# Performance work log

Hardware: AMD Instinct MI355X
Metric: run time of the kernel (lower is better)

Reference implementation:

```python
import jax, jax.numpy as jnp
import numpy as np

HIDDEN = 1024
HEADS = 16
HEAD_DIM = HIDDEN // HEADS
B, T = 4, 2048


def setup_inputs() -> dict:
    key = jax.random.key(0)
    k_x, k_w1, k_b1, k_w2, k_b2 = jax.random.split(key, 5)
    lim1 = 1.0 / np.sqrt(HIDDEN)
    x = jax.random.normal(k_x, (B, T, HIDDEN), dtype=jnp.float32)
    # causal lower-triangular mask, broadcastable to [B, H, T, T]
    mask = jnp.tril(jnp.ones((T, T), dtype=jnp.int32))[None, None, :, :]
    # qkv_proj: Linear(HIDDEN, 3*HIDDEN); torch Linear: y = x @ W.T + b
    W_qkv = jax.random.uniform(k_w1, (3 * HIDDEN, HIDDEN), minval=-lim1, maxval=lim1, dtype=jnp.float32)
    b_qkv = jax.random.uniform(k_b1, (3 * HIDDEN,), minval=-lim1, maxval=lim1, dtype=jnp.float32)
    W_out = jax.random.uniform(k_w2, (HIDDEN, HIDDEN), minval=-lim1, maxval=lim1, dtype=jnp.float32)
    b_out = jax.random.uniform(k_b2, (HIDDEN,), minval=-lim1, maxval=lim1, dtype=jnp.float32)
    return {"x": x, "mask": mask, "W_qkv": W_qkv, "b_qkv": b_qkv, "W_out": W_out, "b_out": b_out}


def reference(x, mask, W_qkv, b_qkv, W_out, b_out):
    Bx, Tx, C = x.shape
    qkv = x @ W_qkv.T + b_qkv                      # [B, T, 3C]
    qkv = qkv.reshape(Bx, Tx, 3, HEADS, HEAD_DIM)
    qkv = jnp.transpose(qkv, (2, 0, 3, 1, 4))      # [3, B, H, T, Dh]
    Q, K, V = qkv[0], qkv[1], qkv[2]
    scale = 1.0 / np.sqrt(HEAD_DIM)
    scores = jnp.einsum('bhqd,bhkd->bhqk', Q, K) * scale  # [B, H, T, T]
    scores = jnp.where(mask == 0, -jnp.inf, scores)
    probs = jax.nn.softmax(scores, axis=-1)
    ctx = jnp.einsum('bhqk,bhkd->bhqd', probs, V)  # [B, H, T, Dh]
    ctx = jnp.transpose(ctx, (0, 2, 1, 3)).reshape(Bx, Tx, C)
    return ctx @ W_out.T + b_out
```

## Files before the change

kernel.cpp:

```cpp
#include <hip/hip_runtime.h>
#include <cstdint>
#include <cstddef>

#define B_ 4
#define T_ 2048
#define C_ 1024
#define H_ 16
#define D_ 64

typedef __attribute__((ext_vector_type(8))) __bf16 bf16x8;
typedef __attribute__((ext_vector_type(4))) float floatx4;

#define QSCL (0.125f * 1.44269504088896f)
#define FMAX 24.0f

__device__ __forceinline__ unsigned short f2bf(float f) {
  union { float f; unsigned int u; } v; v.f = f;
  unsigned int r = v.u + 0x7fffu + ((v.u >> 16) & 1u);
  return (unsigned short)(r >> 16);
}
__device__ __forceinline__ ushort4 pk4(float a, float b, float c, float d) {
  ushort4 u; u.x = f2bf(a); u.y = f2bf(b); u.z = f2bf(c); u.w = f2bf(d);
  return u;
}
__device__ __forceinline__ bf16x8 cvt8(float4 a, float4 b) {
  bf16x8 r;
  r[0] = a.x; r[1] = a.y; r[2] = a.z; r[3] = a.w;
  r[4] = b.x; r[5] = b.y; r[6] = b.z; r[7] = b.w;
  return r;
}
__device__ __forceinline__ ushort4 pk4c(float a, float b, float c, float d) {
  union { __bf16 b4[4]; ushort4 u; } w;
  w.b4[0] = (__bf16)a; w.b4[1] = (__bf16)b; w.b4[2] = (__bf16)c; w.b4[3] = (__bf16)d;
  return w.u;
}

__device__ __forceinline__ void gl_lds16(const void* g, void* l) {
  __builtin_amdgcn_global_load_lds(
      (const __attribute__((address_space(1))) unsigned int*)g,
      (__attribute__((address_space(3))) unsigned int*)l, 16, 0, 0);
}

__global__ __launch_bounds__(256)
void conv_bf16(const float* __restrict__ src, unsigned short* __restrict__ dst,
               int n8) {
  for (int i = blockIdx.x * 256 + threadIdx.x; i < n8; i += gridDim.x * 256) {
    const float4* s = (const float4*)src + 2 * (size_t)i;
    float4 a = s[0], b = s[1];
    ((bf16x8*)dst)[i] = cvt8(a, b);
  }
}

__global__ __launch_bounds__(256)
void conv_tri(const float* __restrict__ s1, unsigned short* __restrict__ d1, int n1,
              const float* __restrict__ s2, unsigned short* __restrict__ d2, int n2,
              const float* __restrict__ s3, unsigned short* __restrict__ d3, int n3) {
  for (int i = blockIdx.x * 256 + threadIdx.x; i < n1 + n2 + n3; i += gridDim.x * 256) {
    const float4* sp; bf16x8* dp;
    if (i < n1)           { sp = (const float4*)s1 + 2 * (size_t)i;       dp = (bf16x8*)d1 + i; }
    else if (i < n1 + n2) { int j = i - n1;      sp = (const float4*)s2 + 2 * (size_t)j; dp = (bf16x8*)d2 + j; }
    else                  { int j = i - n1 - n2; sp = (const float4*)s3 + 2 * (size_t)j; dp = (bf16x8*)d3 + j; }
    float4 a = sp[0], b = sp[1];
    *dp = cvt8(a, b);
  }
}

template<int EPI, int GATHER, int WBF>
__global__ __launch_bounds__(256, 3)
void gemm_bt(const unsigned short* __restrict__ Abf,
             const void* __restrict__ Wraw,
             const float* __restrict__ bias,
             float* __restrict__ out,
             unsigned short* __restrict__ qws,
             unsigned short* __restrict__ kws,
             unsigned short* __restrict__ vtws)
{
  alignas(16) __shared__ unsigned short As[128 * 64];
  alignas(16) __shared__ unsigned short Bs[WBF ? 128 * 64 : 128 * 72];
  const int tid  = threadIdx.x;
  const int lane = tid & 63;
  const int wid  = tid >> 6;
  const int col  = lane & 15;
  const int quad = lane >> 4;
  const int wm = (wid >> 1) << 6;
  const int wn = (wid & 1) << 6;
  const int bm = blockIdx.y << 7;
  const int bn = blockIdx.x << 7;

  const float* Wf          = (const float*)Wraw;
  const unsigned short* Wb = (const unsigned short*)Wraw;

  const int r0 = tid >> 3;
  const int c0 = tid & 7;

  floatx4 acc[4][4];
#pragma unroll
  for (int i = 0; i < 4; ++i)
#pragma unroll
    for (int j = 0; j < 4; ++j)
      acc[i][j] = (floatx4){0.f, 0.f, 0.f, 0.f};

  for (int k0 = 0; k0 < 1024; k0 += 64) {
    __syncthreads();
#pragma unroll
    for (int s = 0; s < 4; ++s) {
      const int row  = (s << 5) + r0;
      const int colE = ((c0 ^ (row & 7)) << 3);
      const unsigned short* gsrc;
      if (GATHER) {
        const int m = bm + row;
        const int b = m >> 11, t = m & 2047;
        const int h = k0 >> 6;
        gsrc = Abf + ((((size_t)(b * 16 + h) << 11) + t) << 6) + colE;
      } else {
        gsrc = Abf + (size_t)(bm + row) * 1024 + k0 + colE;
      }
      gl_lds16(gsrc, (char*)As + (s << 12) + (wid << 10));
    }
    if (WBF) {
#pragma unroll
      for (int s = 0; s < 4; ++s) {
        const int row  = (s << 5) + r0;
        const int colE = ((c0 ^ (row & 7)) << 3);
        const unsigned short* gsrc = Wb + (size_t)(bn + row) * 1024 + k0 + colE;
        gl_lds16(gsrc, (char*)Bs + (s << 12) + (wid << 10));
      }
    } else {
#pragma unroll
      for (int s = 0; s < 4; ++s) {
        const int row = (s << 5) + r0;
        const int kc  = c0 << 3;
        const float* wsrc = &Wf[(size_t)(bn + row) * 1024 + k0 + kc];
        float4 w0 = *(const float4*)wsrc;
        float4 w1 = *(const float4*)(wsrc + 4);
        *(bf16x8*)&Bs[row * 72 + kc] = cvt8(w0, w1);
      }
    }
    __syncthreads();
#pragma unroll
    for (int kk = 0; kk < 64; kk += 32) {
      bf16x8 af[4], bfr[4];
#pragma unroll
      for (int i = 0; i < 4; ++i) {
        const int r = wm + i * 16 + col;
        af[i] = *(const bf16x8*)&As[(r << 6) + ((kk + quad * 8) ^ ((r & 7) << 3))];
      }
#pragma unroll
      for (int j = 0; j < 4; ++j) {
        const int r = wn + j * 16 + col;
        if (WBF)
          bfr[j] = *(const bf16x8*)&Bs[(r << 6) + ((kk + quad * 8) ^ ((r & 7) << 3))];
        else
          bfr[j] = *(const bf16x8*)&Bs[r * 72 + kk + quad * 8];
      }
#pragma unroll
      for (int i = 0; i < 4; ++i)
#pragma unroll
        for (int j = 0; j < 4; ++j)
          acc[i][j] = __builtin_amdgcn_mfma_f32_16x16x32_bf16(af[i], bfr[j], acc[i][j], 0, 0, 0);
    }
  }

#pragma unroll
  for (int i = 0; i < 4; ++i) {
    const int row = bm + wm + i * 16 + quad * 4;
#pragma unroll
    for (int j = 0; j < 4; ++j) {
      const int n  = bn + wn + j * 16 + col;
      const float bv = bias[n];
      float v[4];
#pragma unroll
      for (int r = 0; r < 4; ++r) v[r] = acc[i][j][r] + bv;

      if (EPI == 1) {
#pragma unroll
        for (int r = 0; r < 4; ++r)
          out[(size_t)(row + r) * 1024 + n] = v[r];
      } else {
        const int s   = n >> 10;
        const int rem = n & 1023;
        const int h   = rem >> 6;
        const int d   = rem & 63;
        const int b   = row >> 11;
        const int t   = row & 2047;
        const size_t bh = (size_t)(b * H_ + h);
        if (s == 0) {
#pragma unroll
          for (int r = 0; r < 4; ++r)
            qws[(bh * T_ + t + r) * D_ + d] = f2bf(v[r] * QSCL);
        } else if (s == 1) {
#pragma unroll
          for (int r = 0; r < 4; ++r)
            kws[(bh * T_ + t + r) * D_ + d] = f2bf(v[r]);
        } else {
          *(ushort4*)&vtws[(bh * D_ + d) * T_ + t] = pk4(v[0], v[1], v[2], v[3]);
        }
      }
    }
  }
}

__global__ __launch_bounds__(256, 3)
void attn_causal(unsigned short* __restrict__ qws,
                 const unsigned short* __restrict__ kws,
                 const unsigned short* __restrict__ vtws)
{
  alignas(16) __shared__ unsigned short Ks[2][64 * 64];
  alignas(16) __shared__ unsigned short Vs[2][64 * 64];
  alignas(16) __shared__ unsigned short Ps[4][2][16][72];
  const int tid  = threadIdx.x;
  const int lane = tid & 63;
  const int wid  = tid >> 6;
  const int col  = lane & 15;
  const int quad = lane >> 4;

  const int bh   = blockIdx.x & 63;
  const int band = 15 - (blockIdx.x >> 6);

  const unsigned short* Kp  = kws + (size_t)bh * T_ * D_;
  const unsigned short* Vtp = vtws + (size_t)bh * D_ * T_;

  bf16x8 vones;
#pragma unroll
  for (int i = 0; i < 8; ++i) vones[i] = (__bf16)1.0f;

  const int srow8 = lane >> 3;
  const int swz   = ((lane & 7) ^ srow8) << 3;

#define STAGE(kt_, b_)                                                        \
  do {                                                                        \
    _Pragma("unroll") for (int c2 = 0; c2 < 2; ++c2) {                        \
      const int cb = wid + (c2 << 2);                   \
      gl_lds16(Kp + ((size_t)(((kt_) << 6) + (cb << 3) + srow8) << 6) + swz,  \
               (char*)&Ks[b_][0] + (cb << 10));                               \
      gl_lds16(Vtp + ((size_t)((cb << 3) + srow8) << 11) + ((kt_) << 6) + swz,\
               (char*)&Vs[b_][0] + (cb << 10));                               \
    }                                                                         \
  } while (0)

  const int nk = (band << 1) + 2;
  const int q0 = (band << 7) + (wid << 5);
  unsigned short* Qp = qws + ((size_t)bh * T_ + q0) * D_;

  bf16x8 bq[2][2];
#pragma unroll
  for (int h = 0; h < 2; ++h) {
    bq[h][0] = *(const bf16x8*)&Qp[(h * 16 + col) * D_ + quad * 8];
    bq[h][1] = *(const bf16x8*)&Qp[(h * 16 + col) * D_ + 32 + quad * 8];
  }

  floatx4 o[2][4], ol[2];
#pragma unroll
  for (int h = 0; h < 2; ++h) {
    ol[h] = (floatx4){0.f, 0.f, 0.f, 0.f};
#pragma unroll
    for (int j = 0; j < 4; ++j) o[h][j] = (floatx4){0.f, 0.f, 0.f, 0.f};
  }

  STAGE(0, 0);
  __syncthreads();

  for (int kt = 0; kt < nk; ++kt) {
    const int buf = kt & 1;
    if (kt + 1 < nk) STAGE(kt + 1, buf ^ 1);

    const unsigned short* Kb = &Ks[buf][0];
    bf16x8 kA[4], kB[4];
#pragma unroll
    for (int g = 0; g < 4; ++g) {
      const int r = g * 16 + col;
      kA[g] = *(const bf16x8*)&Kb[(r << 6) + ((quad ^ (col & 7)) << 3)];
      kB[g] = *(const bf16x8*)&Kb[(r << 6) + (((quad | 4) ^ (col & 7)) << 3)];
    }

    floatx4 s[2][4];
    __builtin_amdgcn_s_setprio(1);
#pragma unroll
    for (int h = 0; h < 2; ++h)
#pragma unroll
      for (int g = 0; g < 4; ++g) {
        s[h][g] = (floatx4){-FMAX, -FMAX, -FMAX, -FMAX};
        s[h][g] = __builtin_amdgcn_mfma_f32_16x16x32_bf16(kA[g], bq[h][0], s[h][g], 0, 0, 0);
        s[h][g] = __builtin_amdgcn_mfma_f32_16x16x32_bf16(kB[g], bq[h][1], s[h][g], 0, 0, 0);
      }
    __builtin_amdgcn_s_setprio(0);

    if (kt >= nk - 2) {
#pragma unroll
      for (int h = 0; h < 2; ++h) {
        const int lim = q0 - (kt << 6) + (h << 4) + col;
#pragma unroll
        for (int g = 0; g < 4; ++g)
#pragma unroll
          for (int r = 0; r < 4; ++r)
            if (g * 16 + quad * 4 + r > lim) s[h][g][r] = -1e30f;
      }
    }

#pragma unroll
    for (int h = 0; h < 2; ++h)
#pragma unroll
      for (int g = 0; g < 4; ++g)
#pragma unroll
        for (int r = 0; r < 4; ++r)
          s[h][g][r] = exp2f(s[h][g][r]);

#pragma unroll
    for (int h = 0; h < 2; ++h)
#pragma unroll
      for (int g = 0; g < 4; ++g)
        *(ushort4*)&Ps[wid][h][col][g * 16 + quad * 4] =
            pk4c(s[h][g][0], s[h][g][1], s[h][g][2], s[h][g][3]);
    asm volatile("s_waitcnt lgkmcnt(0)" ::: "memory");

    const unsigned short* Vb = &Vs[buf][0];
    bf16x8 vA[4], vB[4];
#pragma unroll
    for (int j = 0; j < 4; ++j) {
      const int r = j * 16 + col;
      vA[j] = *(const bf16x8*)&Vb[(r << 6) + ((quad ^ (col & 7)) << 3)];
      vB[j] = *(const bf16x8*)&Vb[(r << 6) + (((quad | 4) ^ (col & 7)) << 3)];
    }

    __builtin_amdgcn_s_setprio(1);
#pragma unroll
    for (int h = 0; h < 2; ++h) {
      const bf16x8 ap0 = *(const bf16x8*)&Ps[wid][h][col][quad * 8];
      const bf16x8 ap1 = *(const bf16x8*)&Ps[wid][h][col][32 + quad * 8];
#pragma unroll
      for (int j = 0; j < 4; ++j) {
        o[h][j] = __builtin_amdgcn_mfma_f32_16x16x32_bf16(ap0, vA[j], o[h][j], 0, 0, 0);
        o[h][j] = __builtin_amdgcn_mfma_f32_16x16x32_bf16(ap1, vB[j], o[h][j], 0, 0, 0);
      }
      ol[h] = __builtin_amdgcn_mfma_f32_16x16x32_bf16(ap0, vones, ol[h], 0, 0, 0);
      ol[h] = __builtin_amdgcn_mfma_f32_16x16x32_bf16(ap1, vones, ol[h], 0, 0, 0);
    }
    __builtin_amdgcn_s_setprio(0);

    __syncthreads();
  }

#pragma unroll
  for (int h = 0; h < 2; ++h) {
    float lr[4];
#pragma unroll
    for (int r = 0; r < 4; ++r) lr[r] = 1.0f / ol[h][r];
#pragma unroll
    for (int j = 0; j < 4; ++j)
#pragma unroll
      for (int r = 0; r < 4; ++r)
        Qp[(size_t)(h * 16 + quad * 4 + r) * D_ + j * 16 + col] =
            f2bf(o[h][j][r] * lr[r]);
  }
#undef STAGE
}

extern "C" void kernel_launch(void* const* d_in, const int* in_sizes, int n_in,
                              void* d_out, int out_size, void* d_ws, size_t ws_size,
                              hipStream_t stream) {
  const float* x     = (const float*)d_in[0];
  const float* W_qkv = (const float*)d_in[2];
  const float* b_qkv = (const float*)d_in[3];
  const float* W_out = (const float*)d_in[4];
  const float* b_out = (const float*)d_in[5];
  float* out = (float*)d_out;

  const size_t per = (size_t)B_ * H_ * T_ * D_;
  unsigned short* qws  = (unsigned short*)d_ws;
  unsigned short* vtws = qws + per;
  unsigned short* kws  = (unsigned short*)d_out;
  unsigned short* xbf  = kws + per;

  const bool bigws  = ws_size >= (size_t)38 * 1024 * 1024;
  const bool hugews = ws_size >= (size_t)40 * 1024 * 1024;
  unsigned short* wqbf = vtws + per;
  unsigned short* wobf = wqbf + (size_t)3 * C_ * C_;

  if (hugews) {
    conv_tri<<<dim3(2048), 256, 0, stream>>>(
        x, xbf, (int)(per >> 3),
        W_qkv, wqbf, (3 * C_ * C_) >> 3,
        W_out, wobf, (C_ * C_) >> 3);
    gemm_bt<0, 0, 1><<<dim3(3072 / 128, 8192 / 128), 256, 0, stream>>>(
        xbf, (const void*)wqbf, b_qkv, nullptr, qws, kws, vtws);
  } else if (bigws) {
    conv_tri<<<dim3(2048), 256, 0, stream>>>(
        x, xbf, (int)(per >> 3),
        W_qkv, wqbf, (3 * C_ * C_) >> 3,
        nullptr, nullptr, 0);
    gemm_bt<0, 0, 1><<<dim3(3072 / 128, 8192 / 128), 256, 0, stream>>>(
        xbf, (const void*)wqbf, b_qkv, nullptr, qws, kws, vtws);
  } else {
    conv_bf16<<<dim3(2048), 256, 0, stream>>>(x, xbf, (int)(per >> 3));
    gemm_bt<0, 0, 0><<<dim3(3072 / 128, 8192 / 128), 256, 0, stream>>>(
        xbf, (const void*)W_qkv, b_qkv, nullptr, qws, kws, vtws);
  }

  attn_causal<<<dim3(16 * 64), 256, 0, stream>>>(qws, kws, vtws);

  if (hugews) {
    gemm_bt<1, 1, 1><<<dim3(1024 / 128, 8192 / 128), 256, 0, stream>>>(
        qws, (const void*)wobf, b_out, out, nullptr, nullptr, nullptr);
  } else {
    conv_bf16<<<dim3(512), 256, 0, stream>>>(W_out, vtws, (C_ * C_) >> 3);
    gemm_bt<1, 1, 1><<<dim3(1024 / 128, 8192 / 128), 256, 0, stream>>>(
        qws, (const void*)vtws, b_out, out, nullptr, nullptr, nullptr);
  }
}
```

Measured before the change: 265.8 us.

## Reshuffle attention probabilities in registers with permlane swaps instead of LDS

Drops the per-wave LDS staging buffer for the softmax probabilities. The P fragment is now rearranged into MFMA A-operand layout directly in registers using permlane32/permlane16 swaps. The change also uses the raw exp2 builtin, moves the V fragment loads ahead of the mask and exp step, and lowers the launch-bounds occupancy hint from 3 to 2 waves per SIMD. It aims to remove LDS write/read round trips and the lgkmcnt wait. The permuted K-ordering must still match V's ordering, and the lower occupancy hint may let the compiler use more registers at the cost of fewer waves in flight.

```diff
diff --git a/kernel.cpp b/kernel.cpp
--- a/kernel.cpp
+++ b/kernel.cpp
@@ -29,9 +29,9 @@
   r[4] = b.x; r[5] = b.y; r[6] = b.z; r[7] = b.w;
   return r;
 }
-__device__ __forceinline__ ushort4 pk4c(float a, float b, float c, float d) {
-  union { __bf16 b4[4]; ushort4 u; } w;
-  w.b4[0] = (__bf16)a; w.b4[1] = (__bf16)b; w.b4[2] = (__bf16)c; w.b4[3] = (__bf16)d;
+__device__ __forceinline__ unsigned pkbf2(float a, float b) {
+  union { __bf16 h[2]; unsigned u; } w;
+  w.h[0] = (__bf16)a; w.h[1] = (__bf16)b;
   return w.u;
 }
 
@@ -200,14 +200,13 @@
   }
 }
 
-__global__ __launch_bounds__(256, 3)
+__global__ __launch_bounds__(256, 2)
 void attn_causal(unsigned short* __restrict__ qws,
                  const unsigned short* __restrict__ kws,
                  const unsigned short* __restrict__ vtws)
 {
   alignas(16) __shared__ unsigned short Ks[2][64 * 64];
   alignas(16) __shared__ unsigned short Vs[2][64 * 64];
-  alignas(16) __shared__ unsigned short Ps[4][2][16][72];
   const int tid  = threadIdx.x;
   const int lane = tid & 63;
   const int wid  = tid >> 6;
@@ -285,34 +284,6 @@
       }
     __builtin_amdgcn_s_setprio(0);
 
-    if (kt >= nk - 2) {
-#pragma unroll
-      for (int h = 0; h < 2; ++h) {
-        const int lim = q0 - (kt << 6) + (h << 4) + col;
-#pragma unroll
-        for (int g = 0; g < 4; ++g)
-#pragma unroll
-          for (int r = 0; r < 4; ++r)
-            if (g * 16 + quad * 4 + r > lim) s[h][g][r] = -1e30f;
-      }
-    }
-
-#pragma unroll
-    for (int h = 0; h < 2; ++h)
-#pragma unroll
-      for (int g = 0; g < 4; ++g)
-#pragma unroll
-        for (int r = 0; r < 4; ++r)
-          s[h][g][r] = exp2f(s[h][g][r]);
-
-#pragma unroll
-    for (int h = 0; h < 2; ++h)
-#pragma unroll
-      for (int g = 0; g < 4; ++g)
-        *(ushort4*)&Ps[wid][h][col][g * 16 + quad * 4] =
-            pk4c(s[h][g][0], s[h][g][1], s[h][g][2], s[h][g][3]);
-    asm volatile("s_waitcnt lgkmcnt(0)" ::: "memory");
-
     const unsigned short* Vb = &Vs[buf][0];
     bf16x8 vA[4], vB[4];
 #pragma unroll
@@ -322,18 +293,67 @@
       vB[j] = *(const bf16x8*)&Vb[(r << 6) + (((quad | 4) ^ (col & 7)) << 3)];
     }
 
+    if (kt >= nk - 2) {
+#pragma unroll
+      for (int h = 0; h < 2; ++h) {
+        const int lim = q0 - (kt << 6) + (h << 4) + col;
+#pragma unroll
+        for (int g = 0; g < 4; ++g)
+#pragma unroll
+          for (int r = 0; r < 4; ++r)
+            if (g * 16 + quad * 4 + r > lim) s[h][g][r] = -1e30f;
+      }
+    }
+
+#pragma unroll
+    for (int h = 0; h < 2; ++h)
+#pragma unroll
+      for (int g = 0; g < 4; ++g)
+#pragma unroll
+        for (int r = 0; r < 4; ++r)
+          s[h][g][r] = __builtin_amdgcn_exp2f(s[h][g][r]);
+
     __builtin_amdgcn_s_setprio(1);
 #pragma unroll
     for (int h = 0; h < 2; ++h) {
-      const bf16x8 ap0 = *(const bf16x8*)&Ps[wid][h][col][quad * 8];
-      const bf16x8 ap1 = *(const bf16x8*)&Ps[wid][h][col][32 + quad * 8];
+      unsigned dw[4][2];
+#pragma unroll
+      for (int g = 0; g < 4; ++g) {
+        dw[g][0] = pkbf2(s[h][g][0], s[h][g][1]);
+        dw[g][1] = pkbf2(s[h][g][2], s[h][g][3]);
+      }
+      unsigned aw[4], bw[4];
+      {
+        auto t = __builtin_amdgcn_permlane32_swap(dw[0][0], dw[1][0], false, false);
+        auto u = __builtin_amdgcn_permlane16_swap(t[0], t[1], false, false);
+        aw[0] = u[0]; aw[2] = u[1];
+      }
+      {
+        auto t = __builtin_amdgcn_permlane32_swap(dw[0][1], dw[1][1], false, false);
+        auto u = __builtin_amdgcn_permlane16_swap(t[0], t[1], false, false);
+        aw[1] = u[0]; aw[3] = u[1];
+      }
+      {
+        auto t = __builtin_amdgcn_permlane32_swap(dw[2][0], dw[3][0], false, false);
+        auto u = __builtin_amdgcn_permlane16_swap(t[0], t[1], false, false);
+        bw[0] = u[0]; bw[2] = u[1];
+      }
+      {
+        auto t = __builtin_amdgcn_permlane32_swap(dw[2][1], dw[3][1], false, false);
+        auto u = __builtin_amdgcn_permlane16_swap(t[0], t[1], false, false);
+        bw[1] = u[0]; bw[3] = u[1];
+      }
+      union { unsigned u[4]; bf16x8 v; } pa0, pa1;
+#pragma unroll
+      for (int w = 0; w < 4; ++w) { pa0.u[w] = aw[w]; pa1.u[w] = bw[w]; }
+
 #pragma unroll
       for (int j = 0; j < 4; ++j) {
-        o[h][j] = __builtin_amdgcn_mfma_f32_16x16x32_bf16(ap0, vA[j], o[h][j], 0, 0, 0);
-        o[h][j] = __builtin_amdgcn_mfma_f32_16x16x32_bf16(ap1, vB[j], o[h][j], 0, 0, 0);
-      }
-      ol[h] = __builtin_amdgcn_mfma_f32_16x16x32_bf16(ap0, vones, ol[h], 0, 0, 0);
-      ol[h] = __builtin_amdgcn_mfma_f32_16x16x32_bf16(ap1, vones, ol[h], 0, 0, 0);
+        o[h][j] = __builtin_amdgcn_mfma_f32_16x16x32_bf16(pa0.v, vA[j], o[h][j], 0, 0, 0);
+        o[h][j] = __builtin_amdgcn_mfma_f32_16x16x32_bf16(pa1.v, vB[j], o[h][j], 0, 0, 0);
+      }
+      ol[h] = __builtin_amdgcn_mfma_f32_16x16x32_bf16(pa0.v, vones, ol[h], 0, 0, 0);
+      ol[h] = __builtin_amdgcn_mfma_f32_16x16x32_bf16(pa1.v, vones, ol[h], 0, 0, 0);
     }
     __builtin_amdgcn_s_setprio(0);
 
```

New measurement: 245.0 us. -7.8%, faster.
